# Kernel optimization log

Measured on AMD Instinct MI355X. Metric: run time of the kernel, lower is better.

Reference implementation:

```python
import jax, jax.numpy as jnp
import numpy as np
from jax import lax

B, C, H, W = 16, 128, 192, 192
KEY_POINTS = 512


def setup_inputs() -> dict:
    key = jax.random.key(0)
    ks = jax.random.split(key, 7)
    features = jax.random.normal(ks[0], (B, C, H, W), dtype=jnp.float32)
    # SimpleAttention: Conv2d(C, C, 1) -> weight [C, C], bias [C]
    attn_w = jax.random.normal(ks[1], (C, C), dtype=jnp.float32) * (1.0 / np.sqrt(C))
    attn_b = jnp.zeros((C,), dtype=jnp.float32)
    # Conv2d(C, 64, 3, padding=1)
    conv1_w = jax.random.normal(ks[2], (64, C, 3, 3), dtype=jnp.float32) * (1.0 / np.sqrt(C * 9))
    conv1_b = jnp.zeros((64,), dtype=jnp.float32)
    # Conv2d(64, 2, 1)
    conv2_w = jax.random.normal(ks[3], (2, 64), dtype=jnp.float32) * (1.0 / np.sqrt(64))
    conv2_b = jnp.zeros((2,), dtype=jnp.float32)
    return {
        "features": features,
        "attn_w": attn_w,
        "attn_b": attn_b,
        "conv1_w": conv1_w,
        "conv1_b": conv1_b,
        "conv2_w": conv2_w,
        "conv2_b": conv2_b,
    }


def _forward(features, attn_w, attn_b, conv1_w, conv1_b, conv2_w, conv2_b):
    b, c, h, w = features.shape
    # SimpleAttention: global avg pool -> 1x1 conv -> sigmoid -> scale
    pool = jnp.mean(features, axis=(2, 3))                       # [B, C]
    attn = jax.nn.sigmoid(pool @ attn_w.T + attn_b)               # [B, C]
    x = features * attn[:, :, None, None]                        # [B, C, H, W]
    # Conv2d(C, 64, 3, padding=1) + GELU (exact, torch default)
    y = lax.conv_general_dilated(
        x, conv1_w, window_strides=(1, 1), padding=((1, 1), (1, 1)),
        dimension_numbers=("NCHW", "OIHW", "NCHW"))
    y = jax.nn.gelu(y + conv1_b[None, :, None, None], approximate=False)
    # Conv2d(64, 2, 1)
    sparse_output = jnp.einsum("bchw,oc->bohw", y, conv2_w) + conv2_b[None, :, None, None]
    depth_pred = sparse_output[:, 0:1]                            # [B, 1, H, W]
    confidence = sparse_output[:, 1:2]                            # [B, 1, H, W]
    # softmax over flattened spatial dims
    confidence = jax.nn.softmax(confidence.reshape(b, -1), axis=1).reshape(b, 1, h, w)
    # avg_pool2d(k=3, s=1, p=1) with count_include_pad=True (torch default): divide by 9
    confidence = lax.reduce_window(
        confidence, 0.0, lax.add, (1, 1, 3, 3), (1, 1, 1, 1),
        ((0, 0), (0, 0), (1, 1), (1, 1))) / 9.0
    conf_flat = confidence.reshape(b, -1)                         # [B, H*W]
    depth_flat = depth_pred.reshape(b, -1)                        # [B, H*W]
    k = min(KEY_POINTS, h * w)
    _, indices = lax.top_k(conf_flat, k)                          # [B, k]
    sparse_depths = jnp.take_along_axis(depth_flat, indices, axis=1)  # [B, k]
    y_idx = (indices // w).astype(jnp.float32) / h
    x_idx = (indices % w).astype(jnp.float32) / w
    sparse_points = jnp.stack([x_idx, y_idx, sparse_depths], axis=2)  # [B, k, 3]
    return sparse_points, depth_pred, confidence


def reference(features, attn_w, attn_b, conv1_w, conv1_b, conv2_w, conv2_b):
    return _forward(features, attn_w, attn_b, conv1_w, conv1_b, conv2_w, conv2_b)
```

## Files before the change

### kernel.cpp

```cpp
#include <hip/hip_runtime.h>
#include <math.h>

#define BATCH 16
#define CIN   128
#define HH    192
#define WW    192
#define HW    (HH*WW)
#define OC    64
#define KPTS  512
#define CAP   2048
#define UMAX  (CAP*9)
#define LBLK  768
#define PPB   8
#define NXB   (HW/64)

typedef short short8 __attribute__((ext_vector_type(8)));
typedef float f32x4 __attribute__((ext_vector_type(4)));

__device__ __forceinline__ unsigned short rne_bf16(float v) {
  unsigned u = __float_as_uint(v);
  u += 0x7FFFu + ((u >> 16) & 1u);
  return (unsigned short)(u >> 16);
}

__global__ __launch_bounds__(256) void xq_kernel(const float* __restrict__ feat,
                                                 float* __restrict__ xq,
                                                 double* __restrict__ psum,
                                                 int b0) {
  __shared__ float lds[64*130];
  const int bl = blockIdx.y;
  const int b  = b0 + bl;
  const int px0 = blockIdx.x * 64;
  const int tid = threadIdx.x;
  const int lane = tid & 63, wq = tid >> 6;

  #pragma unroll 8
  for (int k = 0; k < 32; k++) {
    int c = wq + 4*k;
    lds[lane*130 + c] = feat[((size_t)(b*CIN + c))*HW + px0 + lane];
  }
  __syncthreads();

  if (tid < CIN) {
    double s = 0.0;
    #pragma unroll 8
    for (int px = 0; px < 64; px++) s += (double)lds[px*130 + tid];
    psum[((size_t)b*CIN + tid)*NXB + blockIdx.x] = s;
  }

  const int px = tid >> 2, cq = tid & 3;
  size_t base = ((size_t)bl*HW + px0 + px)*CIN + cq*32;
  float4* xqp = (float4*)(xq + base);
  #pragma unroll
  for (int half = 0; half < 8; half++) {
    float4 q;
    #pragma unroll
    for (int j = 0; j < 4; j++)
      ((float*)&q)[j] = lds[px*130 + cq*32 + half*4 + j];
    xqp[half] = q;
  }
}

__global__ __launch_bounds__(64) void poolreduce_kernel(const double* __restrict__ psum,
                                                        double* __restrict__ pool,
                                                        int b0) {
  const int lb = blockIdx.x / CIN, c = blockIdx.x % CIN;
  const int b = b0 + lb;
  const int tid = threadIdx.x;
  const double* pp = psum + ((size_t)b*CIN + c)*NXB;
  double s = 0.0;
  for (int j = tid; j < NXB; j += 64) s += pp[j];
  for (int off = 32; off > 0; off >>= 1) s += __shfl_down(s, off, 64);
  if (tid == 0) pool[b*CIN + c] = s / 36864.0;
}

__global__ __launch_bounds__(128) void attn_kernel(const double* __restrict__ pool,
                                                   const float* __restrict__ attn_w,
                                                   const float* __restrict__ attn_b,
                                                   double* __restrict__ attn_d,
                                                   float* __restrict__ attn_f,
                                                   int b0) {
  __shared__ double sp[CIN];
  int b = b0 + blockIdx.x, c = threadIdx.x;
  sp[c] = pool[b*CIN + c];
  __syncthreads();
  double s = (double)attn_b[c];
  const float* wr = attn_w + (size_t)c * CIN;
  for (int j = 0; j < CIN; j++) s = fma((double)wr[j], sp[j], s);
  double a = 1.0 / (1.0 + exp(-s));
  attn_d[b*CIN + c] = a;
  attn_f[b*CIN + c] = (float)a;
}

__global__ __launch_bounds__(256) void wtrans_kernel(const float* __restrict__ w,
                                                     unsigned short* __restrict__ wb_h,
                                                     unsigned short* __restrict__ wb_l) {
  int i = blockIdx.x * 256 + threadIdx.x;
  if (i < OC*CIN*9) {
    int oc = i / (CIN*9);
    int r  = i % (CIN*9);
    int c  = r / 9;
    int k  = r % 9;
    float v = w[i];
    unsigned short h = rne_bf16(v);
    float hf = __uint_as_float((unsigned)h << 16);
    wb_h[((size_t)k*OC + oc)*CIN + c] = h;
    wb_l[((size_t)k*OC + oc)*CIN + c] = rne_bf16(v - hf);
  }
}

__global__ __launch_bounds__(256) void wscale64_kernel(const float* __restrict__ w,
                                                       const double* __restrict__ attn_d,
                                                       double* __restrict__ wab64p,
                                                       int b0) {
  const int b = b0 + blockIdx.y;
  int i = blockIdx.x * 256 + threadIdx.x;
  if (i < CIN*OC*10) {
    int kk = i % 10;
    int co = i / 10;
    int oc = co & 63, c = co >> 6;
    double v = 0.0;
    if (kk < 9) v = (double)w[((size_t)oc*CIN + c)*9 + kk] * attn_d[b*CIN + c];
    wab64p[(((size_t)b*CIN + c)*OC + oc)*10 + kk] = v;
  }
}

#define TLH 18
#define TLW 18
#define CST 36
__global__ __launch_bounds__(256, 3) void conv_kernel(const float* __restrict__ xq,
                                                      const float* __restrict__ attn_f,
                                                      const unsigned short* __restrict__ wb_h,
                                                      const unsigned short* __restrict__ wb_l,
                                                      const float* __restrict__ conv1_b,
                                                      const float* __restrict__ conv2_w,
                                                      const float* __restrict__ conv2_b,
                                                      float* __restrict__ depth_out,
                                                      float* __restrict__ logit_out,
                                                      int b0, int nwg) {
  int bid = blockIdx.x;
  int q = nwg >> 3, r = nwg & 7;
  int xcd = bid & 7, pos = bid >> 3;
  int swz = (xcd < r ? xcd*(q+1) : r*(q+1) + (xcd - r)*q) + pos;
  const int bl = swz / 144;
  const int t144 = swz % 144;
  const int b  = b0 + bl;
  const int h0 = (t144 / 12) * 16, w0 = (t144 % 12) * 16;
  const int tid = threadIdx.x;
  const int wv = tid >> 6, ln = tid & 63;
  const int lg = ln >> 4, lr = ln & 15;

  __shared__ __align__(16) unsigned short th[TLH*TLW*CST];
  __shared__ __align__(16) unsigned short tl[TLH*TLW*CST];
  __shared__ float s_attn[CIN];

  if (tid < CIN) s_attn[tid] = attn_f[b*CIN + tid];

  f32x4 acc[4][4];
  #pragma unroll
  for (int mi = 0; mi < 4; mi++)
    #pragma unroll
    for (int ni = 0; ni < 4; ni++)
      acc[mi][ni] = (f32x4){0.f, 0.f, 0.f, 0.f};

  const short8 zero8 = (short8){0,0,0,0,0,0,0,0};

  #pragma unroll 1
  for (int c0 = 0; c0 < CIN; c0 += 32) {
    __syncthreads();
    for (int i = tid; i < TLH*TLW*4; i += 256) {
      int rr  = i / (TLW*4);
      int rw  = i % (TLW*4);
      int col = rw >> 2, sub = rw & 3;
      int gh = h0 + rr - 1, gw = w0 + col - 1;
      short8 hv = zero8, lv = zero8;
      if (gh >= 0 && gh < HH && gw >= 0 && gw < WW) {
        const float4* src = (const float4*)(xq
            + ((size_t)(bl*HH + gh)*WW + gw)*CIN + c0 + sub*8);
        float4 f0 = src[0], f1 = src[1];
        #pragma unroll
        for (int j = 0; j < 8; j++) {
          float raw = (j < 4) ? ((const float*)&f0)[j] : ((const float*)&f1)[j-4];
          float v = raw * s_attn[c0 + sub*8 + j];
          unsigned short h = rne_bf16(v);
          hv[j] = (short)h;
          lv[j] = (short)rne_bf16(v - __uint_as_float((unsigned)h << 16));
        }
      }
      int off = (rr*TLW + col)*CST + sub*8;
      *reinterpret_cast<short8*>(&th[off]) = hv;
      *reinterpret_cast<short8*>(&tl[off]) = lv;
    }
    __syncthreads();

    #pragma unroll
    for (int v = 0; v < 3; v++) {
      short8 ah[6], al[6];
      #pragma unroll
      for (int r6 = 0; r6 < 6; r6++) {
        int off = ((4*wv + r6)*TLW + lr + v)*CST + 8*lg;
        ah[r6] = *reinterpret_cast<const short8*>(&th[off]);
        al[r6] = *reinterpret_cast<const short8*>(&tl[off]);
      }
      #pragma unroll
      for (int u = 0; u < 3; u++) {
        short8 bh[4], blo[4];
        #pragma unroll
        for (int ni = 0; ni < 4; ni++) {
          size_t woff = ((size_t)(u*3 + v)*OC + ni*16 + lr)*CIN + c0 + 8*lg;
          bh[ni]  = *reinterpret_cast<const short8*>(wb_h + woff);
          blo[ni] = *reinterpret_cast<const short8*>(wb_l + woff);
        }
        #pragma unroll
        for (int mi = 0; mi < 4; mi++) {
          #pragma unroll
          for (int ni = 0; ni < 4; ni++) {
            acc[mi][ni] = __builtin_amdgcn_mfma_f32_16x16x32_bf16(ah[mi+u], bh[ni],  acc[mi][ni], 0, 0, 0);
            acc[mi][ni] = __builtin_amdgcn_mfma_f32_16x16x32_bf16(ah[mi+u], blo[ni], acc[mi][ni], 0, 0, 0);
            acc[mi][ni] = __builtin_amdgcn_mfma_f32_16x16x32_bf16(al[mi+u], bh[ni],  acc[mi][ni], 0, 0, 0);
          }
        }
      }
    }
  }

  float bia[4], w20[4], w21[4];
  #pragma unroll
  for (int ni = 0; ni < 4; ni++) {
    int oc = ni*16 + lr;
    bia[ni] = conv1_b[oc];
    w20[ni] = conv2_w[oc];
    w21[ni] = conv2_w[OC + oc];
  }
  const float c2b0 = conv2_b[0], c2b1 = conv2_b[1];

  #pragma unroll
  for (int mi = 0; mi < 4; mi++) {
    const int gh = h0 + 4*wv + mi;
    #pragma unroll
    for (int q2 = 0; q2 < 4; q2++) {
      float s0 = 0.f, s1 = 0.f;
      #pragma unroll
      for (int ni = 0; ni < 4; ni++) {
        float z = acc[mi][ni][q2] + bia[ni];
        float g = 0.5f * z * (1.0f + erff(z * 0.70710678118654752f));
        s0 = fmaf(g, w20[ni], s0);
        s1 = fmaf(g, w21[ni], s1);
      }
      #pragma unroll
      for (int m = 1; m <= 8; m <<= 1) {
        s0 += __shfl_xor(s0, m, 64);
        s1 += __shfl_xor(s1, m, 64);
      }
      if (lr == 0) {
        const int gw = w0 + 4*lg + q2;
        depth_out[((size_t)b*HH + gh)*WW + gw] = s0 + c2b0;
        logit_out[((size_t)b*HH + gh)*WW + gw] = s1 + c2b1;
      }
    }
  }
}

__global__ __launch_bounds__(1024) void softmax_kernel(float* __restrict__ logits,
                                                       float* __restrict__ m_out,
                                                       int b0) {
  const int b = b0 + blockIdx.x;
  float* lp = logits + (size_t)b * HW;
  const int tid = threadIdx.x;
  __shared__ float sred[16];
  __shared__ float s_m, s_z;

  float m = -INFINITY;
  for (int i = tid; i < HW; i += 1024) m = fmaxf(m, lp[i]);
  for (int off = 32; off > 0; off >>= 1) m = fmaxf(m, __shfl_down(m, off, 64));
  if ((tid & 63) == 0) sred[tid >> 6] = m;
  __syncthreads();
  if (tid == 0) {
    float t = sred[0];
    for (int i = 1; i < 16; i++) t = fmaxf(t, sred[i]);
    s_m = t;
    m_out[b] = t;
  }
  __syncthreads();
  m = s_m;

  float z = 0.f;
  for (int i = tid; i < HW; i += 1024) z += expf(lp[i] - m);
  __syncthreads();
  for (int off = 32; off > 0; off >>= 1) z += __shfl_down(z, off, 64);
  if ((tid & 63) == 0) sred[tid >> 6] = z;
  __syncthreads();
  if (tid == 0) {
    float t = 0.f;
    for (int i = 0; i < 16; i++) t += sred[i];
    s_z = t;
  }
  __syncthreads();
  z = s_z;

  for (int i = tid; i < HW; i += 1024) lp[i] = expf(lp[i] - m) / z;
}

__global__ __launch_bounds__(256) void box_kernel(const float* __restrict__ p,
                                                  float* __restrict__ out_f,
                                                  int b0, int g) {
  int i = blockIdx.x * 256 + threadIdx.x;
  if (i >= g * HW) return;
  int b = b0 + i / HW, r = i % HW, h = r / WW, w = r % WW;
  const float* bp = p + (size_t)b * HW;
  float s = 0.f;
  for (int dy = -1; dy <= 1; dy++) {
    int h2 = h + dy;
    if (h2 < 0 || h2 >= HH) continue;
    for (int dx = -1; dx <= 1; dx++) {
      int w2 = w + dx;
      if (w2 < 0 || w2 >= WW) continue;
      s += bp[h2*WW + w2];
    }
  }
  out_f[(size_t)b*HW + r] = s / 9.0f;
}

__global__ __launch_bounds__(1024) void cand_kernel(const float* __restrict__ conf,
                                                    int* __restrict__ cand_idx,
                                                    int* __restrict__ cand_cnt,
                                                    int* __restrict__ upix,
                                                    int* __restrict__ upix_cnt,
                                                    int b0) {
  const int b = b0 + blockIdx.x;
  const float* cp = conf + (size_t)b * HW;
  const int tid = threadIdx.x;
  __shared__ unsigned sred[16];
  __shared__ unsigned s_total;
  __shared__ unsigned s_cnt;
  __shared__ unsigned bm[1152];
  __shared__ unsigned pcs[1152];
  __shared__ unsigned grpoff[37];

  unsigned lo = 0u, hi = 0x7F800000u;
  while (hi - lo > 1u) {
    unsigned mid = lo + ((hi - lo) >> 1);
    unsigned cnt = 0;
    for (int i = tid; i < HW; i += 1024)
      cnt += (__float_as_uint(cp[i]) >= mid) ? 1u : 0u;
    for (int off = 32; off > 0; off >>= 1) cnt += __shfl_down(cnt, off, 64);
    if ((tid & 63) == 0) sred[tid >> 6] = cnt;
    __syncthreads();
    if (tid == 0) {
      unsigned t = 0;
      for (int i = 0; i < 16; i++) t += sred[i];
      s_total = t;
    }
    __syncthreads();
    unsigned total = s_total;
    __syncthreads();
    if (total >= KPTS) lo = mid; else hi = mid;
  }
  float vcut = __uint_as_float(lo) * (1.0f - 1e-4f);

  if (tid == 0) s_cnt = 0;
  for (int i = tid; i < 1152; i += 1024) bm[i] = 0u;
  __syncthreads();

  for (int i = tid; i < HW; i += 1024) {
    if (cp[i] >= vcut) {
      unsigned s = atomicAdd(&s_cnt, 1u);
      if (s < CAP) {
        cand_idx[b*CAP + s] = i;
        int h = i / WW, w = i % WW;
        for (int dy = -1; dy <= 1; dy++) {
          int qh = h + dy;
          if (qh < 0 || qh >= HH) continue;
          for (int dx = -1; dx <= 1; dx++) {
            int qw = w + dx;
            if (qw < 0 || qw >= WW) continue;
            int q = qh*WW + qw;
            atomicOr(&bm[q >> 5], 1u << (q & 31));
          }
        }
      }
    }
  }
  __syncthreads();
  if (tid == 0) cand_cnt[b] = (s_cnt < CAP) ? s_cnt : CAP;

  for (int i = tid; i < 1152; i += 1024) pcs[i] = __popc(bm[i]);
  __syncthreads();
  if (tid < 36) {
    unsigned s = 0;
    for (int j = 0; j < 32; j++) s += pcs[tid*32 + j];
    grpoff[tid] = s;
  }
  __syncthreads();
  if (tid == 0) {
    unsigned run = 0;
    for (int g2 = 0; g2 < 36; g2++) { unsigned t = grpoff[g2]; grpoff[g2] = run; run += t; }
    grpoff[36] = run;
    upix_cnt[b] = (int)run;
  }
  __syncthreads();
  for (int i = tid; i < 1152; i += 1024) {
    unsigned off = grpoff[i >> 5];
    for (int w = (i & ~31); w < i; w++) off += pcs[w];
    unsigned u = bm[i];
    while (u) {
      int bit = __ffs(u) - 1;
      u &= u - 1u;
      upix[b*UMAX + off++] = i*32 + bit;
    }
  }
}

__global__ __launch_bounds__(256) void logit_kernel(const float* __restrict__ xq,
                                                    const double* __restrict__ wab64p,
                                                    const float* __restrict__ conv1_b,
                                                    const float* __restrict__ conv2_w,
                                                    const float* __restrict__ conv2_b,
                                                    const int* __restrict__ upix,
                                                    const int* __restrict__ upix_cnt,
                                                    double* __restrict__ lmap,
                                                    int b0, int nb) {
  int bid = blockIdx.x;
  int swz = (bid & 7) * (nb >> 3) + (bid >> 3);
  const int bl = swz / LBLK;
  const int b  = b0 + bl;
  const int slot0 = swz % LBLK;
  const int ucnt = upix_cnt[b];
  const int tid = threadIdx.x;

  __shared__ __align__(16) float xf[PPB][1536];
  __shared__ double part[4][PPB][64];
  __shared__ int    s_pix[PPB];

  for (int base = slot0*PPB; base < ucnt; base += LBLK*PPB) {
    const int rem = min(PPB, ucnt - base);
    if (tid < PPB) s_pix[tid] = (tid < rem) ? upix[b*UMAX + base + tid] : 0;
    __syncthreads();

    for (int i = tid; i < PPB*9*32; i += 256) {
      int p = i / 288;
      int r = i % 288;
      int k = r >> 5, t = r & 31;
      float4 v = (float4){0.f, 0.f, 0.f, 0.f};
      if (p < rem) {
        int pix = s_pix[p];
        int gh = pix / WW + k/3 - 1, gw = pix % WW + k%3 - 1;
        if (gh >= 0 && gh < HH && gw >= 0 && gw < WW)
          v = *reinterpret_cast<const float4*>(
                xq + ((size_t)(bl*HW + gh*WW + gw))*CIN + 4*t);
      }
      int cb = 4*t;
      xf[p][(cb+0)*12 + k] = v.x;
      xf[p][(cb+1)*12 + k] = v.y;
      xf[p][(cb+2)*12 + k] = v.z;
      xf[p][(cb+3)*12 + k] = v.w;
    }
    __syncthreads();

    const int oc = tid & 63, cq = tid >> 6;
    double acc[PPB];
    #pragma unroll
    for (int p = 0; p < PPB; p++) acc[p] = 0.0;
    const double* wp = wab64p + (((size_t)b*CIN + cq*32)*OC + oc)*10;
    for (int cc = 0; cc < 32; cc++) {
      const int c = cq*32 + cc;
      double2 wv[5];
      #pragma unroll
      for (int q = 0; q < 5; q++) wv[q] = *((const double2*)wp + q);
      wp += OC*10;
      #pragma unroll
      for (int p = 0; p < PPB; p++) {
        const float4* xp = (const float4*)&xf[p][c*12];
        float4 a = xp[0], bb = xp[1], cc4 = xp[2];
        double t = acc[p];
        t = fma(wv[0].x, (double)a.x,  t);
        t = fma(wv[0].y, (double)a.y,  t);
        t = fma(wv[1].x, (double)a.z,  t);
        t = fma(wv[1].y, (double)a.w,  t);
        t = fma(wv[2].x, (double)bb.x, t);
        t = fma(wv[2].y, (double)bb.y, t);
        t = fma(wv[3].x, (double)bb.z, t);
        t = fma(wv[3].y, (double)bb.w, t);
        t = fma(wv[4].x, (double)cc4.x, t);
        acc[p] = t;
      }
    }
    #pragma unroll
    for (int p = 0; p < PPB; p++) part[cq][p][oc] = acc[p];
    __syncthreads();

    for (int t0 = tid; t0 < PPB*64; t0 += 256) {
      const int p = t0 >> 6, o = t0 & 63;
      double z = part[0][p][o] + part[1][p][o] + part[2][p][o] + part[3][p][o]
               + (double)conv1_b[o];
      double g = 0.5 * z * (1.0 + erf(z * 0.70710678118654752440));
      double cv = g * (double)conv2_w[OC + o];
      #pragma unroll
      for (int m = 1; m <= 32; m <<= 1) cv += __shfl_xor(cv, m, 64);
      if (o == 0 && p < rem)
        lmap[(size_t)b*HW + s_pix[p]] = cv + (double)conv2_b[1];
    }
    __syncthreads();
  }
}

__global__ __launch_bounds__(256) void score_kernel(const double* __restrict__ lmap,
                                                    const float* __restrict__ m32,
                                                    const int* __restrict__ cand_idx,
                                                    const int* __restrict__ cand_cnt,
                                                    double* __restrict__ cand_score,
                                                    int b0) {
  const int b = b0 + blockIdx.y;
  const int slot = blockIdx.x * 256 + threadIdx.x;
  if (slot >= cand_cnt[b]) return;
  const int idx = cand_idx[b*CAP + slot];
  const int ph = idx / WW, pw = idx % WW;
  const double m = (double)m32[b];
  double s = 0.0;
  for (int dy = -1; dy <= 1; dy++) {
    int qh = ph + dy;
    if (qh < 0 || qh >= HH) continue;
    for (int dx = -1; dx <= 1; dx++) {
      int qw = pw + dx;
      if (qw < 0 || qw >= WW) continue;
      s += exp(lmap[(size_t)b*HW + qh*WW + qw] - m);
    }
  }
  cand_score[b*CAP + slot] = s;
}

__global__ __launch_bounds__(1024) void emit_kernel(const double* __restrict__ cand_score,
                                                    const int* __restrict__ cand_idx,
                                                    const int* __restrict__ cand_cnt,
                                                    const float* __restrict__ depth,
                                                    float* __restrict__ points,
                                                    int b0) {
  const int b = b0 + blockIdx.x;
  const int tid = threadIdx.x;
  __shared__ double vals[CAP];
  __shared__ int    idxs[CAP];

  int cnt = cand_cnt[b];
  for (int i = tid; i < CAP; i += 1024) {
    if (i < cnt) { vals[i] = cand_score[b*CAP + i]; idxs[i] = cand_idx[b*CAP + i]; }
    else         { vals[i] = -1.0;                  idxs[i] = 0x7FFFFFFF; }
  }
  __syncthreads();

  for (unsigned k = 2; k <= CAP; k <<= 1) {
    for (unsigned j = k >> 1; j > 0; j >>= 1) {
      unsigned t = (unsigned)tid;
      unsigned i1 = ((t & ~(j - 1u)) << 1) | (t & (j - 1u));
      unsigned i2 = i1 | j;
      double v1 = vals[i1], v2 = vals[i2];
      int    a1 = idxs[i1], a2 = idxs[i2];
      bool oneAfterTwo = (v1 < v2) || (v1 == v2 && a1 > a2);
      bool descSeg = ((i1 & k) == 0);
      if (descSeg ? oneAfterTwo : !oneAfterTwo) {
        vals[i1] = v2; idxs[i1] = a2;
        vals[i2] = v1; idxs[i2] = a1;
      }
      __syncthreads();
    }
  }

  if (tid < KPTS) {
    int idx = idxs[tid];
    float d = depth[(size_t)b * HW + idx];
    float xi = (float)(idx % WW) / (float)WW;
    float yi = (float)(idx / WW) / (float)HH;
    float* pp = points + ((size_t)b * KPTS + tid) * 3;
    pp[0] = xi; pp[1] = yi; pp[2] = d;
  }
}

extern "C" void kernel_launch(void* const* d_in, const int* in_sizes, int n_in,
                              void* d_out, int out_size, void* d_ws, size_t ws_size,
                              hipStream_t stream) {
  const float* feat    = (const float*)d_in[0];
  const float* attn_w  = (const float*)d_in[1];
  const float* attn_b  = (const float*)d_in[2];
  const float* conv1_w = (const float*)d_in[3];
  const float* conv1_b = (const float*)d_in[4];
  const float* conv2_w = (const float*)d_in[5];
  const float* conv2_b = (const float*)d_in[6];

  float* out    = (float*)d_out;
  float* points = out;
  float* depth  = out + 24576;
  float* conf_f = out + 24576 + BATCH*HW;

  double* wsd        = (double*)d_ws;
  double* pool_d     = wsd;
  double* attn_d     = wsd + 2048;
  double* cand_score = wsd + 4096;
  double* lmap       = cand_score + BATCH*CAP;
  double* wab64p     = lmap + (size_t)BATCH*HW;
  double* psum       = wab64p + (size_t)BATCH*CIN*OC*10;
  float*  wsf        = (float*)(psum + (size_t)BATCH*CIN*NXB);
  float*  logit32    = wsf;
  float*  attn_f     = logit32 + (size_t)BATCH*HW;
  float*  m32        = attn_f + 2048;
  unsigned short* wb_h = (unsigned short*)(m32 + 16);
  unsigned short* wb_l = wb_h + OC*CIN*9;
  int*    cand_idx   = (int*)(wb_l + OC*CIN*9);
  int*    cand_cnt   = cand_idx + BATCH*CAP;
  int*    upix       = cand_cnt + 16;
  int*    upix_cnt   = upix + BATCH*UMAX;
  size_t fixed_bytes = ((size_t)((char*)(upix_cnt + 16) - (char*)d_ws) + 255) & ~(size_t)255;
  char* dyn_base = (char*)d_ws + fixed_bytes;
  const size_t pbe = (size_t)HW * CIN;
  const size_t per_batch_bytes = pbe * 4;
  size_t avail = (ws_size > fixed_bytes + 65536) ? (ws_size - fixed_bytes - 65536) : 0;
  int gb = (int)(avail / per_batch_bytes);
  if (gb > BATCH) gb = BATCH;
  if (gb < 1) gb = 1;
  float* xq = (float*)dyn_base;

  wtrans_kernel<<<(OC*CIN*9 + 255)/256, 256, 0, stream>>>(conv1_w, wb_h, wb_l);

  for (int b0 = 0; b0 < BATCH; b0 += gb) {
    int g = (BATCH - b0 < gb) ? (BATCH - b0) : gb;
    xq_kernel<<<dim3(NXB, g), 256, 0, stream>>>(feat, xq, psum, b0);
    poolreduce_kernel<<<g*CIN, 64, 0, stream>>>(psum, pool_d, b0);
    attn_kernel<<<g, CIN, 0, stream>>>(pool_d, attn_w, attn_b, attn_d, attn_f, b0);
    wscale64_kernel<<<dim3((CIN*OC*10 + 255)/256, g), 256, 0, stream>>>(conv1_w, attn_d,
                                                                        wab64p, b0);
    conv_kernel<<<g*144, 256, 0, stream>>>(xq, attn_f, wb_h, wb_l,
                                           conv1_b, conv2_w, conv2_b,
                                           depth, logit32, b0, g*144);
    softmax_kernel<<<g, 1024, 0, stream>>>(logit32, m32, b0);
    box_kernel<<<(g*HW + 255)/256, 256, 0, stream>>>(logit32, conf_f, b0, g);
    cand_kernel<<<g, 1024, 0, stream>>>(conf_f, cand_idx, cand_cnt, upix, upix_cnt, b0);
    logit_kernel<<<g*LBLK, 256, 0, stream>>>(xq, wab64p, conv1_b, conv2_w, conv2_b,
                                             upix, upix_cnt, lmap, b0, g*LBLK);
    score_kernel<<<dim3(CAP/256, g), 256, 0, stream>>>(lmap, m32, cand_idx, cand_cnt,
                                                       cand_score, b0);
    emit_kernel<<<g, 1024, 0, stream>>>(cand_score, cand_idx, cand_cnt, depth, points, b0);
  }
}
```

Measured before the change: 947.3 us.

## Prefetch next channel chunk of input tile into registers during MFMA compute

The per-iteration tile loading loop is unrolled into six fixed work units whose addresses and bounds checks are computed once before the channel loop. Global loads for half of the units for the next 32-channel chunk are issued after the barrier so they overlap with the MFMA compute of the current chunk. The remaining units still load synchronously. This hides part of the global load latency and removes repeated index math, at the cost of extra registers in a kernel already bounded to three blocks per CU.

After: 1.263 ms. 33.3% more time.

```diff
diff --git a/kernel.cpp b/kernel.cpp
--- a/kernel.cpp
+++ b/kernel.cpp
@@ -123,6 +123,40 @@
     if (kk < 9) v = (double)w[((size_t)oc*CIN + c)*9 + kk] * attn_d[b*CIN + c];
     wab64p[(((size_t)b*CIN + c)*OC + oc)*10 + kk] = v;
   }
+}
+
+__device__ __forceinline__ void cvt1(float raw, float a,
+                                     unsigned short &h, unsigned short &l) {
+  float v = raw * a;
+  h = rne_bf16(v);
+  l = rne_bf16(v - __uint_as_float((unsigned)h << 16));
+}
+
+__device__ __forceinline__ void cvt_store(float4 A, float4 B, const float* at,
+                                          unsigned short* thp, unsigned short* tlp) {
+  short8 hv, lv; unsigned short h, l;
+  cvt1(A.x, at[0], h, l); hv[0]=(short)h; lv[0]=(short)l;
+  cvt1(A.y, at[1], h, l); hv[1]=(short)h; lv[1]=(short)l;
+  cvt1(A.z, at[2], h, l); hv[2]=(short)h; lv[2]=(short)l;
+  cvt1(A.w, at[3], h, l); hv[3]=(short)h; lv[3]=(short)l;
+  cvt1(B.x, at[4], h, l); hv[4]=(short)h; lv[4]=(short)l;
+  cvt1(B.y, at[5], h, l); hv[5]=(short)h; lv[5]=(short)l;
+  cvt1(B.z, at[6], h, l); hv[6]=(short)h; lv[6]=(short)l;
+  cvt1(B.w, at[7], h, l); hv[7]=(short)h; lv[7]=(short)l;
+  *reinterpret_cast<short8*>(thp) = hv;
+  *reinterpret_cast<short8*>(tlp) = lv;
+}
+
+__device__ __forceinline__ void load_cvt_store(bool val, const float* up, int c0,
+                                               const float* at,
+                                               unsigned short* thp, unsigned short* tlp) {
+  const float4 zf = (float4){0.f, 0.f, 0.f, 0.f};
+  float4 A = zf, B = zf;
+  if (val) {
+    A = *(const float4*)(up + c0);
+    B = *(const float4*)(up + c0 + 4);
+  }
+  cvt_store(A, B, at, thp, tlp);
 }
 
 #define TLH 18
@@ -156,6 +190,24 @@
 
   if (tid < CIN) s_attn[tid] = attn_f[b*CIN + tid];
 
+#define UNITDEF(n, ioff)                                                     \
+  const int i##n = tid + (ioff);                                             \
+  const int rr##n = i##n / (TLW*4), rw##n = i##n % (TLW*4);                  \
+  const int col##n = rw##n >> 2, s##n = (rw##n & 3) * 8;                     \
+  const int gh##n = h0 + rr##n - 1, gw##n = w0 + col##n - 1;                 \
+  const bool val##n = (gh##n >= 0) && (gh##n < HH) && (gw##n >= 0) && (gw##n < WW); \
+  const float* up##n = xq + ((size_t)(bl*HH + gh##n)*WW + gw##n)*CIN + s##n; \
+  const int o##n = (rr##n*TLW + col##n)*CST + s##n;
+
+  UNITDEF(0, 0)
+  UNITDEF(1, 256)
+  UNITDEF(2, 512)
+  UNITDEF(3, 768)
+  UNITDEF(4, 1024)
+  UNITDEF(5, 1280)
+#undef UNITDEF
+  const bool u5ok = (i5 < TLH*TLW*4);
+
   f32x4 acc[4][4];
   #pragma unroll
   for (int mi = 0; mi < 4; mi++)
@@ -163,35 +215,32 @@
     for (int ni = 0; ni < 4; ni++)
       acc[mi][ni] = (f32x4){0.f, 0.f, 0.f, 0.f};
 
-  const short8 zero8 = (short8){0,0,0,0,0,0,0,0};
+  const float4 zf = (float4){0.f, 0.f, 0.f, 0.f};
+  float4 pa0, pb0, pa1, pb1, pa2, pb2;
+
+#define ISSUE(c0v)                                                           \
+  pa0 = val0 ? *(const float4*)(up0 + (c0v))     : zf;                       \
+  pb0 = val0 ? *(const float4*)(up0 + (c0v) + 4) : zf;                       \
+  pa1 = val1 ? *(const float4*)(up1 + (c0v))     : zf;                       \
+  pb1 = val1 ? *(const float4*)(up1 + (c0v) + 4) : zf;                       \
+  pa2 = val2 ? *(const float4*)(up2 + (c0v))     : zf;                       \
+  pb2 = val2 ? *(const float4*)(up2 + (c0v) + 4) : zf;
+
+  ISSUE(0)
 
   #pragma unroll 1
   for (int c0 = 0; c0 < CIN; c0 += 32) {
     __syncthreads();
-    for (int i = tid; i < TLH*TLW*4; i += 256) {
-      int rr  = i / (TLW*4);
-      int rw  = i % (TLW*4);
-      int col = rw >> 2, sub = rw & 3;
-      int gh = h0 + rr - 1, gw = w0 + col - 1;
-      short8 hv = zero8, lv = zero8;
-      if (gh >= 0 && gh < HH && gw >= 0 && gw < WW) {
-        const float4* src = (const float4*)(xq
-            + ((size_t)(bl*HH + gh)*WW + gw)*CIN + c0 + sub*8);
-        float4 f0 = src[0], f1 = src[1];
-        #pragma unroll
-        for (int j = 0; j < 8; j++) {
-          float raw = (j < 4) ? ((const float*)&f0)[j] : ((const float*)&f1)[j-4];
-          float v = raw * s_attn[c0 + sub*8 + j];
-          unsigned short h = rne_bf16(v);
-          hv[j] = (short)h;
-          lv[j] = (short)rne_bf16(v - __uint_as_float((unsigned)h << 16));
-        }
-      }
-      int off = (rr*TLW + col)*CST + sub*8;
-      *reinterpret_cast<short8*>(&th[off]) = hv;
-      *reinterpret_cast<short8*>(&tl[off]) = lv;
-    }
-    __syncthreads();
+    cvt_store(pa0, pb0, &s_attn[c0 + s0], &th[o0], &tl[o0]);
+    cvt_store(pa1, pb1, &s_attn[c0 + s1], &th[o1], &tl[o1]);
+    cvt_store(pa2, pb2, &s_attn[c0 + s2], &th[o2], &tl[o2]);
+    load_cvt_store(val3, up3, c0, &s_attn[c0 + s3], &th[o3], &tl[o3]);
+    load_cvt_store(val4, up4, c0, &s_attn[c0 + s4], &th[o4], &tl[o4]);
+    if (u5ok)
+      load_cvt_store(val5, up5, c0, &s_attn[c0 + s5], &th[o5], &tl[o5]);
+    __syncthreads();
+
+    if (c0 + 32 < CIN) { ISSUE(c0 + 32) }
 
     #pragma unroll
     for (int v = 0; v < 3; v++) {
@@ -223,6 +272,7 @@
       }
     }
   }
+#undef ISSUE
 
   float bia[4], w20[4], w21[4];
   #pragma unroll
@@ -239,23 +289,23 @@
     const int gh = h0 + 4*wv + mi;
     #pragma unroll
     for (int q2 = 0; q2 < 4; q2++) {
-      float s0 = 0.f, s1 = 0.f;
+      float s0v = 0.f, s1v = 0.f;
       #pragma unroll
       for (int ni = 0; ni < 4; ni++) {
         float z = acc[mi][ni][q2] + bia[ni];
         float g = 0.5f * z * (1.0f + erff(z * 0.70710678118654752f));
-        s0 = fmaf(g, w20[ni], s0);
-        s1 = fmaf(g, w21[ni], s1);
+        s0v = fmaf(g, w20[ni], s0v);
+        s1v = fmaf(g, w21[ni], s1v);
       }
       #pragma unroll
       for (int m = 1; m <= 8; m <<= 1) {
-        s0 += __shfl_xor(s0, m, 64);
-        s1 += __shfl_xor(s1, m, 64);
+        s0v += __shfl_xor(s0v, m, 64);
+        s1v += __shfl_xor(s1v, m, 64);
       }
       if (lr == 0) {
         const int gw = w0 + 4*lg + q2;
-        depth_out[((size_t)b*HH + gh)*WW + gw] = s0 + c2b0;
-        logit_out[((size_t)b*HH + gh)*WW + gw] = s1 + c2b1;
+        depth_out[((size_t)b*HH + gh)*WW + gw] = s0v + c2b0;
+        logit_out[((size_t)b*HH + gh)*WW + gw] = s1v + c2b1;
       }
     }
   }
```
